# Kernel optimization log

Measured on AMD Instinct MI355X. Metric: run time of the kernel, lower is better.

The kernel has to match this reference:

```python
import jax, jax.numpy as jnp
import numpy as np

N_NODES = 50000


def gcn_conv(x, src, dst, W, b, n_nodes):
    """PyG-style GCNConv: x' = D^-1/2 (A + I) D^-1/2 (x W) + b.
    src/dst already include self-loops."""
    h = x @ W  # [N, C_out]
    # symmetric normalization from degree (with self-loops, unit edge weight)
    deg = jax.ops.segment_sum(jnp.ones_like(dst, dtype=h.dtype), dst,
                              num_segments=n_nodes)  # [N]
    dinv = jnp.where(deg > 0, jax.lax.rsqrt(deg), 0.0)
    norm = dinv[src] * dinv[dst]  # [E]
    msg = h[src] * norm[:, None]  # gather + scale, [E, C_out]
    out = jax.ops.segment_sum(msg, dst, num_segments=n_nodes)  # scatter-add
    return out + b


def setup_inputs() -> dict:
    key = jax.random.key(0)
    k1, k2, k3, k4, k5, k6 = jax.random.split(key, 6)
    in_c, hid_c, out_c = 128, 64, 64
    x = jax.random.normal(k1, (N_NODES, in_c), dtype=jnp.float32)
    edge_index = jax.random.randint(k2, (2, 800000), 0, N_NODES, dtype=jnp.int64)
    # Glorot-ish init for weights, zeros for bias (as PyG default)
    W1 = jax.random.normal(k3, (in_c, hid_c), dtype=jnp.float32) / np.sqrt(in_c)
    b1 = jnp.zeros((hid_c,), dtype=jnp.float32)
    W2 = jax.random.normal(k4, (hid_c, out_c), dtype=jnp.float32) / np.sqrt(hid_c)
    b2 = jnp.zeros((out_c,), dtype=jnp.float32)
    return {"x": x, "edge_index": edge_index, "W1": W1, "b1": b1,
            "W2": W2, "b2": b2}


def reference(x, edge_index, W1, b1, W2, b2):
    n = x.shape[0]
    loops = jnp.arange(n, dtype=edge_index.dtype)
    src = jnp.concatenate([edge_index[0], loops])  # add self-loops
    dst = jnp.concatenate([edge_index[1], loops])
    h = gcn_conv(x, src, dst, W1, b1, n)
    h = jax.nn.relu(h)
    return gcn_conv(h, src, dst, W2, b2, n)
```

## Files before the change

### kernel.cpp

```cpp
#include <hip/hip_runtime.h>
#include <hip/hip_fp16.h>


#define C_HID 64

static inline size_t alignup(size_t x) { return (x + 255) & ~(size_t)255; }

typedef __attribute__((address_space(3))) unsigned int lds_uint;
typedef __attribute__((address_space(1))) const unsigned int glob_uint;

__device__ __forceinline__ int blockScanIncl256(int v, int* wsum) {
    const int lane = threadIdx.x & 63, wav = threadIdx.x >> 6;
    int s = v;
#pragma unroll
    for (int off = 1; off < 64; off <<= 1) {
        int t = __shfl_up(s, off);
        if (lane >= off) s += t;
    }
    if (lane == 63) wsum[wav] = s;
    __syncthreads();
    if (wav == 0 && lane < 4) {
        int ws = wsum[lane];
#pragma unroll
        for (int off = 1; off < 4; off <<= 1) {
            int t = __shfl_up(ws, off);
            if (lane >= off) ws += t;
        }
        wsum[lane] = ws;
    }
    __syncthreads();
    return (wav ? wsum[wav - 1] : 0) + s;
}

template <int K>
__global__ __launch_bounds__(256) void gemm1_hist_kernel(
    const float* __restrict__ X, const float* __restrict__ W,
    const int* __restrict__ dst, __half* __restrict__ outh,
    int* __restrict__ S, int n, int E, int ePer, int nb) {
    constexpr int KP = K + 4;
    __shared__ float Xs[64 * KP];
    __shared__ float Ws[K * 64];
    __shared__ int h[256];
    const int t = threadIdx.x;
    const int lane = t & 63;
    const int wav = t >> 6;

    if ((int)blockIdx.x < nb) {
        h[t] = 0;
        __syncthreads();
        int beg = blockIdx.x * ePer, end = min(E, beg + ePer);
        for (int e = beg + t; e < end; e += 256)
            atomicAdd(&h[dst[e] >> 8], 1);
        __syncthreads();
        for (int b = t; b < nb; b += 256)
            S[(size_t)b * nb + blockIdx.x] = h[b];
        return;
    }

    const int row0 = ((int)blockIdx.x - nb) * 64;
    {
        const char* gb = (const char*)W;
        char* lb = (char*)Ws;
        for (int off = wav * 1024; off < K * 64 * 4; off += 4096)
            __builtin_amdgcn_global_load_lds((glob_uint*)(gb + off + lane * 16),
                                             (lds_uint*)(lb + off), 16, 0, 0);
    }
    if (row0 + 64 <= n) {
        const float4* g4 = (const float4*)(X + (size_t)row0 * K);
        for (int i = t; i < 64 * (K / 4); i += 256) {
            float4 v = g4[i];
            int r = i / (K / 4), k0 = (i % (K / 4)) * 4;
            *(float4*)&Xs[r * KP + k0] = v;
        }
    } else {
        for (int i = t; i < 64 * K; i += 256) {
            int r = i / K, k = i % K;
            Xs[r * KP + k] = (row0 + r < n) ? X[(size_t)(row0 + r) * K + k] : 0.0f;
        }
    }
    __syncthreads();

    const int tx = t & 15;
    const int ty = t >> 4;
    float acc[4][4] = {{0.f}};
#pragma unroll 2
    for (int k0 = 0; k0 < K; k0 += 4) {
        float4 a0 = *(const float4*)&Xs[(4 * ty + 0) * KP + k0];
        float4 a1 = *(const float4*)&Xs[(4 * ty + 1) * KP + k0];
        float4 a2 = *(const float4*)&Xs[(4 * ty + 2) * KP + k0];
        float4 a3 = *(const float4*)&Xs[(4 * ty + 3) * KP + k0];
        float4 b0 = *(const float4*)&Ws[(k0 + 0) * 64 + 4 * tx];
        float4 b1 = *(const float4*)&Ws[(k0 + 1) * 64 + 4 * tx];
        float4 b2 = *(const float4*)&Ws[(k0 + 2) * 64 + 4 * tx];
        float4 b3 = *(const float4*)&Ws[(k0 + 3) * 64 + 4 * tx];
        const float* ap[4] = {(const float*)&a0, (const float*)&a1,
                              (const float*)&a2, (const float*)&a3};
        const float* bp[4] = {(const float*)&b0, (const float*)&b1,
                              (const float*)&b2, (const float*)&b3};
#pragma unroll
        for (int r = 0; r < 4; ++r)
#pragma unroll
            for (int kk = 0; kk < 4; ++kk) {
                float av = ap[r][kk];
#pragma unroll
                for (int c = 0; c < 4; ++c)
                    acc[r][c] = fmaf(av, bp[kk][c], acc[r][c]);
            }
    }
#pragma unroll
    for (int r = 0; r < 4; ++r) {
        int row = row0 + 4 * ty + r;
        if (row < n) {
            __half2 p01 = __floats2half2_rn(acc[r][0], acc[r][1]);
            __half2 p23 = __floats2half2_rn(acc[r][2], acc[r][3]);
            float2 st;
            ((__half2*)&st)[0] = p01;
            ((__half2*)&st)[1] = p23;
            *(float2*)&outh[(size_t)row * 64 + 4 * tx] = st;
        }
    }
}

__global__ __launch_bounds__(256) void scan_rows_kernel(
    int* __restrict__ S, int* __restrict__ T, int nb) {
    __shared__ int wsum[4];
    const int b = blockIdx.x, t = threadIdx.x;
    int v = (t < nb) ? S[(size_t)b * nb + t] : 0;
    int incl = blockScanIncl256(v, wsum);
    if (t < nb) S[(size_t)b * nb + t] = incl - v;
    if (t == 0) T[b] = wsum[3];
}

__global__ __launch_bounds__(256) void scan_T_kernel(int* __restrict__ T, int nb) {
    __shared__ int wsum[4];
    const int t = threadIdx.x;
    int v = (t < nb) ? T[t] : 0;
    int incl = blockScanIncl256(v, wsum);
    if (t < nb) T[t] = incl - v;
    if (t == nb - 1) T[nb] = incl;
}

__global__ __launch_bounds__(256) void scatter_kernel(
    const int* __restrict__ src, const int* __restrict__ dst, int E, int ePer,
    const int* __restrict__ S, const int* __restrict__ T,
    unsigned* __restrict__ ebuf, int nb) {
    __shared__ int arr[256];
    const int b = blockIdx.x, t = threadIdx.x;
    if (t < nb) arr[t] = S[(size_t)t * nb + b] + T[t];
    __syncthreads();
    int beg = b * ePer, end = min(E, beg + ePer);
    for (int e = beg + t; e < end; e += 256) {
        int d = dst[e];
        int s = src[e];
        int pos = atomicAdd(&arr[d >> 8], 1);
        ebuf[pos] = ((unsigned)s << 8) | (unsigned)(d & 255);
    }
}

__global__ __launch_bounds__(256) void build_kernel(
    const unsigned* __restrict__ ebuf, const int* __restrict__ T,
    int* __restrict__ row_ptr, float* __restrict__ dinv,
    int* __restrict__ esrc, int n, int nb) {
    __shared__ int arr[256];
    __shared__ int wsum[4];
    const int b = blockIdx.x, t = threadIdx.x;
    const int node0 = b << 8;
    const int ebeg = T[b];
    const int eend = T[b + 1];

    arr[t] = 0;
    __syncthreads();
    for (int e = ebeg + t; e < eend; e += 256)
        atomicAdd(&arr[ebuf[e] & 255], 1);
    __syncthreads();
    int deg = arr[t];
    int incl = blockScanIncl256(deg, wsum);
    int excl = incl - deg;
    __syncthreads();
    arr[t] = ebeg + excl;
    int v = node0 + t;
    if (v < n) {
        row_ptr[v + 1] = ebeg + incl;
        dinv[v] = rsqrtf(1.0f + (float)deg);
        if (v == 0) row_ptr[0] = 0;
    }
    __syncthreads();
    for (int e = ebeg + t; e < eend; e += 256) {
        unsigned p = ebuf[e];
        int pos = atomicAdd(&arr[p & 255], 1);
        esrc[pos] = (int)(p >> 8);
    }
}

__global__ __launch_bounds__(256) void agg1_gemm2_kernel(
    const __half* __restrict__ g1, const int* __restrict__ row_ptr,
    const int* __restrict__ esrc, const float* __restrict__ dinv,
    const float* __restrict__ b1, const float* __restrict__ W2,
    __half* __restrict__ g2, int n) {
    __shared__ float Bt[64][68];
    __shared__ float Ws2[64 * 64];
    const int t = threadIdx.x, lane = t & 63, wav = t >> 6;

    {
        const char* gb = (const char*)W2;
        char* lb = (char*)Ws2;
        for (int off = wav * 1024; off < 64 * 64 * 4; off += 4096)
            __builtin_amdgcn_global_load_lds((glob_uint*)(gb + off + lane * 16),
                                             (lds_uint*)(lb + off), 16, 0, 0);
    }

    const int g = t >> 2;
    const int c = t & 3;
    const int row0 = blockIdx.x * 64;
    const int v = row0 + g;
    const float4* __restrict__ hs4 = (const float4*)g1;

    if (v < n) {
        float acc[16];
        float dv0 = dinv[v];
        {
            size_t rb = (size_t)v * 8 + 2 * c;
            float4 r0 = hs4[rb], r1 = hs4[rb + 1];
            const __half2* h0 = (const __half2*)&r0;
            const __half2* h1 = (const __half2*)&r1;
#pragma unroll
            for (int q = 0; q < 4; ++q) {
                float2 f0 = __half22float2(h0[q]);
                float2 f1 = __half22float2(h1[q]);
                acc[2 * q] = f0.x * dv0;     acc[2 * q + 1] = f0.y * dv0;
                acc[8 + 2 * q] = f1.x * dv0; acc[9 + 2 * q] = f1.y * dv0;
            }
        }
        const int beg = row_ptr[v], end = row_ptr[v + 1];
        int j = beg;
        for (; j + 2 <= end; j += 2) {
            int s0 = esrc[j], s1 = esrc[j + 1];
            float d0 = dinv[s0], d1 = dinv[s1];
            size_t rb0 = (size_t)s0 * 8 + 2 * c, rb1 = (size_t)s1 * 8 + 2 * c;
            float4 a0 = hs4[rb0], a1 = hs4[rb0 + 1];
            float4 e0 = hs4[rb1], e1 = hs4[rb1 + 1];
            const __half2* pa0 = (const __half2*)&a0;
            const __half2* pa1 = (const __half2*)&a1;
            const __half2* pe0 = (const __half2*)&e0;
            const __half2* pe1 = (const __half2*)&e1;
#pragma unroll
            for (int q = 0; q < 4; ++q) {
                float2 f;
                f = __half22float2(pa0[q]);
                acc[2 * q] = fmaf(f.x, d0, acc[2 * q]);
                acc[2 * q + 1] = fmaf(f.y, d0, acc[2 * q + 1]);
                f = __half22float2(pa1[q]);
                acc[8 + 2 * q] = fmaf(f.x, d0, acc[8 + 2 * q]);
                acc[9 + 2 * q] = fmaf(f.y, d0, acc[9 + 2 * q]);
                f = __half22float2(pe0[q]);
                acc[2 * q] = fmaf(f.x, d1, acc[2 * q]);
                acc[2 * q + 1] = fmaf(f.y, d1, acc[2 * q + 1]);
                f = __half22float2(pe1[q]);
                acc[8 + 2 * q] = fmaf(f.x, d1, acc[8 + 2 * q]);
                acc[9 + 2 * q] = fmaf(f.y, d1, acc[9 + 2 * q]);
            }
        }
        if (j < end) {
            int s0 = esrc[j];
            float d0 = dinv[s0];
            size_t rb0 = (size_t)s0 * 8 + 2 * c;
            float4 a0 = hs4[rb0], a1 = hs4[rb0 + 1];
            const __half2* pa0 = (const __half2*)&a0;
            const __half2* pa1 = (const __half2*)&a1;
#pragma unroll
            for (int q = 0; q < 4; ++q) {
                float2 f;
                f = __half22float2(pa0[q]);
                acc[2 * q] = fmaf(f.x, d0, acc[2 * q]);
                acc[2 * q + 1] = fmaf(f.y, d0, acc[2 * q + 1]);
                f = __half22float2(pa1[q]);
                acc[8 + 2 * q] = fmaf(f.x, d0, acc[8 + 2 * q]);
                acc[9 + 2 * q] = fmaf(f.y, d0, acc[9 + 2 * q]);
            }
        }
        const float* bb = b1 + c * 16;
#pragma unroll
        for (int u = 0; u < 4; ++u) {
            float4 w;
            w.x = fmaxf(fmaf(acc[4 * u + 0], dv0, bb[4 * u + 0]), 0.f);
            w.y = fmaxf(fmaf(acc[4 * u + 1], dv0, bb[4 * u + 1]), 0.f);
            w.z = fmaxf(fmaf(acc[4 * u + 2], dv0, bb[4 * u + 2]), 0.f);
            w.w = fmaxf(fmaf(acc[4 * u + 3], dv0, bb[4 * u + 3]), 0.f);
            *(float4*)&Bt[g][c * 16 + 4 * u] = w;
        }
    } else {
#pragma unroll
        for (int u = 0; u < 4; ++u)
            *(float4*)&Bt[g][c * 16 + 4 * u] = make_float4(0.f, 0.f, 0.f, 0.f);
    }
    __syncthreads();

    const int tx = t & 15;
    const int ty = t >> 4;
    float a2[4][4] = {{0.f}};
#pragma unroll 2
    for (int k0 = 0; k0 < 64; k0 += 4) {
        float4 x0 = *(const float4*)&Bt[4 * ty + 0][k0];
        float4 x1 = *(const float4*)&Bt[4 * ty + 1][k0];
        float4 x2 = *(const float4*)&Bt[4 * ty + 2][k0];
        float4 x3 = *(const float4*)&Bt[4 * ty + 3][k0];
        float4 w0 = *(const float4*)&Ws2[(k0 + 0) * 64 + 4 * tx];
        float4 w1 = *(const float4*)&Ws2[(k0 + 1) * 64 + 4 * tx];
        float4 w2 = *(const float4*)&Ws2[(k0 + 2) * 64 + 4 * tx];
        float4 w3 = *(const float4*)&Ws2[(k0 + 3) * 64 + 4 * tx];
        const float* xp[4] = {(const float*)&x0, (const float*)&x1,
                              (const float*)&x2, (const float*)&x3};
        const float* wp[4] = {(const float*)&w0, (const float*)&w1,
                              (const float*)&w2, (const float*)&w3};
#pragma unroll
        for (int r = 0; r < 4; ++r)
#pragma unroll
            for (int kk = 0; kk < 4; ++kk) {
                float av = xp[r][kk];
#pragma unroll
                for (int cc = 0; cc < 4; ++cc)
                    a2[r][cc] = fmaf(av, wp[kk][cc], a2[r][cc]);
            }
    }
#pragma unroll
    for (int r = 0; r < 4; ++r) {
        int row = row0 + 4 * ty + r;
        if (row < n) {
            float dv = dinv[row];
            __half2 p01 = __floats2half2_rn(a2[r][0] * dv, a2[r][1] * dv);
            __half2 p23 = __floats2half2_rn(a2[r][2] * dv, a2[r][3] * dv);
            float2 st;
            ((__half2*)&st)[0] = p01;
            ((__half2*)&st)[1] = p23;
            *(float2*)&g2[(size_t)row * 64 + 4 * tx] = st;
        }
    }
}

__global__ __launch_bounds__(256) void aggregate2_kernel(
    const __half* __restrict__ hs,
    const int* __restrict__ row_ptr,
    const int* __restrict__ esrc,
    const float* __restrict__ dinv,
    const float* __restrict__ bias,
    float* __restrict__ out, int n) {
    const int v = blockIdx.x * 32 + (threadIdx.x >> 3);
    if (v >= n) return;
    const int c8 = threadIdx.x & 7;
    const float4* __restrict__ hs4 = (const float4*)hs;

    const int beg = row_ptr[v];
    const int end = row_ptr[v + 1];

    float acc[8];
    {
        float4 raw = hs4[(size_t)v * 8 + c8];
        const __half2* hp = (const __half2*)&raw;
#pragma unroll
        for (int q = 0; q < 4; ++q) {
            float2 f = __half22float2(hp[q]);
            acc[2 * q] = f.x; acc[2 * q + 1] = f.y;
        }
    }

    int j = beg;
    for (; j + 4 <= end; j += 4) {
        int s0 = esrc[j], s1 = esrc[j + 1], s2 = esrc[j + 2], s3 = esrc[j + 3];
        float4 r0 = hs4[(size_t)s0 * 8 + c8];
        float4 r1 = hs4[(size_t)s1 * 8 + c8];
        float4 r2 = hs4[(size_t)s2 * 8 + c8];
        float4 r3 = hs4[(size_t)s3 * 8 + c8];
        const __half2* h0 = (const __half2*)&r0;
        const __half2* h1 = (const __half2*)&r1;
        const __half2* h2 = (const __half2*)&r2;
        const __half2* h3 = (const __half2*)&r3;
#pragma unroll
        for (int q = 0; q < 4; ++q) {
            float2 f0 = __half22float2(h0[q]);
            float2 f1 = __half22float2(h1[q]);
            float2 f2 = __half22float2(h2[q]);
            float2 f3 = __half22float2(h3[q]);
            acc[2 * q]     += (f0.x + f1.x) + (f2.x + f3.x);
            acc[2 * q + 1] += (f0.y + f1.y) + (f2.y + f3.y);
        }
    }
    for (; j < end; ++j) {
        int s0 = esrc[j];
        float4 r0 = hs4[(size_t)s0 * 8 + c8];
        const __half2* h0 = (const __half2*)&r0;
#pragma unroll
        for (int q = 0; q < 4; ++q) {
            float2 f0 = __half22float2(h0[q]);
            acc[2 * q] += f0.x;
            acc[2 * q + 1] += f0.y;
        }
    }

    float dv = dinv[v];
    float4 b0 = *(const float4*)(bias + c8 * 8);
    float4 b1v = *(const float4*)(bias + c8 * 8 + 4);
    float4 o0, o1;
    o0.x = fmaf(acc[0], dv, b0.x); o0.y = fmaf(acc[1], dv, b0.y);
    o0.z = fmaf(acc[2], dv, b0.z); o0.w = fmaf(acc[3], dv, b0.w);
    o1.x = fmaf(acc[4], dv, b1v.x); o1.y = fmaf(acc[5], dv, b1v.y);
    o1.z = fmaf(acc[6], dv, b1v.z); o1.w = fmaf(acc[7], dv, b1v.w);
    float4* op = (float4*)(out + (size_t)v * 64 + c8 * 8);
    op[0] = o0;
    op[1] = o1;
}

extern "C" void kernel_launch(void* const* d_in, const int* in_sizes, int n_in,
                              void* d_out, int out_size, void* d_ws, size_t ws_size,
                              hipStream_t stream) {
    const float* x  = (const float*)d_in[0];
    const int*   ei = (const int*)d_in[1];
    const float* W1 = (const float*)d_in[2];
    const float* b1 = (const float*)d_in[3];
    const float* W2 = (const float*)d_in[4];
    const float* b2 = (const float*)d_in[5];
    float* out = (float*)d_out;

    const int C_IN = 128;
    const int n = in_sizes[0] / C_IN;
    const int E = in_sizes[1] / 2;
    const int* src = ei;
    const int* dst = ei + E;

    const int nb = (n + 255) >> 8;
    const int ngb = (n + 63) / 64;
    const int ePer = (E + nb - 1) / nb;

    char* w = (char*)d_ws;
    float*    dinv    = (float*)w;    w += alignup((size_t)n * sizeof(float));
    __half*   g1      = (__half*)w;   w += alignup((size_t)n * C_HID * sizeof(__half));
    __half*   g2      = (__half*)w;   w += alignup((size_t)n * C_HID * sizeof(__half));
    int*      row_ptr = (int*)w;      w += alignup((size_t)(n + 1) * sizeof(int));
    int*      S       = (int*)w;      w += alignup((size_t)nb * nb * sizeof(int));
    int*      T       = (int*)w;      w += alignup((size_t)(nb + 1) * sizeof(int));
    unsigned* ebuf    = (unsigned*)w; w += alignup((size_t)E * sizeof(unsigned));
    int*      esrc    = (int*)w;

    gemm1_hist_kernel<128><<<nb + ngb, 256, 0, stream>>>(
        x, W1, dst, g1, S, n, E, ePer, nb);

    scan_rows_kernel<<<nb, 256, 0, stream>>>(S, T, nb);
    scan_T_kernel<<<1, 256, 0, stream>>>(T, nb);
    scatter_kernel<<<nb, 256, 0, stream>>>(src, dst, E, ePer, S, T, ebuf, nb);
    build_kernel<<<nb, 256, 0, stream>>>(ebuf, T, row_ptr, dinv, esrc, n, nb);

    agg1_gemm2_kernel<<<ngb, 256, 0, stream>>>(
        g1, row_ptr, esrc, dinv, b1, W2, g2, n);

    aggregate2_kernel<<<(n + 31) / 32, 256, 0, stream>>>(
        g2, row_ptr, esrc, dinv, b2, out, n);
}
```

Baseline: 162.4 us.

## Split aggregations into two column-half passes and unfuse layer-2 GEMM

Both neighbor aggregations now run in two passes over half of the feature columns, so each pass's gather set (64 B per node instead of 128 B) is more likely to stay in cache. The fused aggregate+GEMM2 kernel is split into a standalone aggregation writing relu output to an fp16 buffer and a separate GEMM kernel that reads it back. In exchange the change adds extra launches, re-reads edge lists and row pointers in each pass, and adds a round trip through global memory for the intermediate.

Measured after the change: 192.7 us. 18.6% more time.

```diff
diff --git a/kernel.cpp b/kernel.cpp
--- a/kernel.cpp
+++ b/kernel.cpp
@@ -192,134 +192,182 @@
     }
 }
 
-__global__ __launch_bounds__(256) void agg1_gemm2_kernel(
+__global__ __launch_bounds__(256) void agg1_half_kernel(
     const __half* __restrict__ g1, const int* __restrict__ row_ptr,
     const int* __restrict__ esrc, const float* __restrict__ dinv,
-    const float* __restrict__ b1, const float* __restrict__ W2,
-    __half* __restrict__ g2, int n) {
-    __shared__ float Bt[64][68];
-    __shared__ float Ws2[64 * 64];
-    const int t = threadIdx.x, lane = t & 63, wav = t >> 6;
-
+    const float* __restrict__ b1, __half* __restrict__ Bh, int n, int pass) {
+    const int v = blockIdx.x * 32 + (threadIdx.x >> 3);
+    if (v >= n) return;
+    const int c8 = threadIdx.x & 7;
+    const int cidx = pass * 8 + c8;
+    const float2* __restrict__ hs2 = (const float2*)g1;
+
+    float dv = dinv[v];
+    float a0, a1, a2, a3;
     {
-        const char* gb = (const char*)W2;
-        char* lb = (char*)Ws2;
-        for (int off = wav * 1024; off < 64 * 64 * 4; off += 4096)
+        float2 raw = hs2[(size_t)v * 16 + cidx];
+        const __half2* hp = (const __half2*)&raw;
+        float2 f0 = __half22float2(hp[0]), f1 = __half22float2(hp[1]);
+        a0 = f0.x * dv; a1 = f0.y * dv; a2 = f1.x * dv; a3 = f1.y * dv;
+    }
+    const int beg = row_ptr[v], end = row_ptr[v + 1];
+    int j = beg;
+    for (; j + 4 <= end; j += 4) {
+        int s0 = esrc[j], s1 = esrc[j + 1], s2 = esrc[j + 2], s3 = esrc[j + 3];
+        float d0 = dinv[s0], d1 = dinv[s1], d2 = dinv[s2], d3 = dinv[s3];
+        float2 r0 = hs2[(size_t)s0 * 16 + cidx];
+        float2 r1 = hs2[(size_t)s1 * 16 + cidx];
+        float2 r2 = hs2[(size_t)s2 * 16 + cidx];
+        float2 r3 = hs2[(size_t)s3 * 16 + cidx];
+        const __half2* h0 = (const __half2*)&r0;
+        const __half2* h1 = (const __half2*)&r1;
+        const __half2* h2 = (const __half2*)&r2;
+        const __half2* h3 = (const __half2*)&r3;
+        float2 f;
+        f = __half22float2(h0[0]); a0 = fmaf(f.x, d0, a0); a1 = fmaf(f.y, d0, a1);
+        f = __half22float2(h0[1]); a2 = fmaf(f.x, d0, a2); a3 = fmaf(f.y, d0, a3);
+        f = __half22float2(h1[0]); a0 = fmaf(f.x, d1, a0); a1 = fmaf(f.y, d1, a1);
+        f = __half22float2(h1[1]); a2 = fmaf(f.x, d1, a2); a3 = fmaf(f.y, d1, a3);
+        f = __half22float2(h2[0]); a0 = fmaf(f.x, d2, a0); a1 = fmaf(f.y, d2, a1);
+        f = __half22float2(h2[1]); a2 = fmaf(f.x, d2, a2); a3 = fmaf(f.y, d2, a3);
+        f = __half22float2(h3[0]); a0 = fmaf(f.x, d3, a0); a1 = fmaf(f.y, d3, a1);
+        f = __half22float2(h3[1]); a2 = fmaf(f.x, d3, a2); a3 = fmaf(f.y, d3, a3);
+    }
+    for (; j < end; ++j) {
+        int s0 = esrc[j];
+        float d0 = dinv[s0];
+        float2 r0 = hs2[(size_t)s0 * 16 + cidx];
+        const __half2* h0 = (const __half2*)&r0;
+        float2 f;
+        f = __half22float2(h0[0]); a0 = fmaf(f.x, d0, a0); a1 = fmaf(f.y, d0, a1);
+        f = __half22float2(h0[1]); a2 = fmaf(f.x, d0, a2); a3 = fmaf(f.y, d0, a3);
+    }
+    float4 b = *(const float4*)(b1 + cidx * 4);
+    float r0 = fmaxf(fmaf(a0, dv, b.x), 0.f);
+    float r1 = fmaxf(fmaf(a1, dv, b.y), 0.f);
+    float r2 = fmaxf(fmaf(a2, dv, b.z), 0.f);
+    float r3 = fmaxf(fmaf(a3, dv, b.w), 0.f);
+    float2 st;
+    ((__half2*)&st)[0] = __floats2half2_rn(r0, r1);
+    ((__half2*)&st)[1] = __floats2half2_rn(r2, r3);
+    ((float2*)Bh)[(size_t)v * 16 + cidx] = st;
+}
+
+__global__ __launch_bounds__(256) void agg2_half_kernel(
+    const __half* __restrict__ g2, const int* __restrict__ row_ptr,
+    const int* __restrict__ esrc, const float* __restrict__ dinv,
+    const float* __restrict__ b2, float* __restrict__ out, int n, int pass) {
+    const int v = blockIdx.x * 32 + (threadIdx.x >> 3);
+    if (v >= n) return;
+    const int c8 = threadIdx.x & 7;
+    const int cidx = pass * 8 + c8;
+    const float2* __restrict__ hs2 = (const float2*)g2;
+
+    float a0, a1, a2, a3;
+    {
+        float2 raw = hs2[(size_t)v * 16 + cidx];
+        const __half2* hp = (const __half2*)&raw;
+        float2 f0 = __half22float2(hp[0]), f1 = __half22float2(hp[1]);
+        a0 = f0.x; a1 = f0.y; a2 = f1.x; a3 = f1.y;
+    }
+    const int beg = row_ptr[v], end = row_ptr[v + 1];
+    int j = beg;
+    for (; j + 4 <= end; j += 4) {
+        int s0 = esrc[j], s1 = esrc[j + 1], s2 = esrc[j + 2], s3 = esrc[j + 3];
+        float2 r0 = hs2[(size_t)s0 * 16 + cidx];
+        float2 r1 = hs2[(size_t)s1 * 16 + cidx];
+        float2 r2 = hs2[(size_t)s2 * 16 + cidx];
+        float2 r3 = hs2[(size_t)s3 * 16 + cidx];
+        const __half2* h0 = (const __half2*)&r0;
+        const __half2* h1 = (const __half2*)&r1;
+        const __half2* h2 = (const __half2*)&r2;
+        const __half2* h3 = (const __half2*)&r3;
+        float2 f0 = __half22float2(h0[0]), g0 = __half22float2(h0[1]);
+        float2 f1 = __half22float2(h1[0]), g1v = __half22float2(h1[1]);
+        float2 f2 = __half22float2(h2[0]), g2v = __half22float2(h2[1]);
+        float2 f3 = __half22float2(h3[0]), g3 = __half22float2(h3[1]);
+        a0 += (f0.x + f1.x) + (f2.x + f3.x);
+        a1 += (f0.y + f1.y) + (f2.y + f3.y);
+        a2 += (g0.x + g1v.x) + (g2v.x + g3.x);
+        a3 += (g0.y + g1v.y) + (g2v.y + g3.y);
+    }
+    for (; j < end; ++j) {
+        int s0 = esrc[j];
+        float2 r0 = hs2[(size_t)s0 * 16 + cidx];
+        const __half2* h0 = (const __half2*)&r0;
+        float2 f = __half22float2(h0[0]), g = __half22float2(h0[1]);
+        a0 += f.x; a1 += f.y; a2 += g.x; a3 += g.y;
+    }
+    float dv = dinv[v];
+    float4 b = *(const float4*)(b2 + cidx * 4);
+    float4 o;
+    o.x = fmaf(a0, dv, b.x);
+    o.y = fmaf(a1, dv, b.y);
+    o.z = fmaf(a2, dv, b.z);
+    o.w = fmaf(a3, dv, b.w);
+    *(float4*)(out + (size_t)v * 64 + cidx * 4) = o;
+}
+
+__global__ __launch_bounds__(256) void gemm2_h_kernel(
+    const __half* __restrict__ Xh, const float* __restrict__ W,
+    const float* __restrict__ dinv, __half* __restrict__ outh, int n) {
+    constexpr int K = 64, KP = 68;
+    __shared__ float Xs[64 * KP];
+    __shared__ float Ws[K * 64];
+    const int t = threadIdx.x;
+    const int lane = t & 63;
+    const int wav = t >> 6;
+    const int row0 = blockIdx.x * 64;
+
+    {
+        const char* gb = (const char*)W;
+        char* lb = (char*)Ws;
+        for (int off = wav * 1024; off < K * 64 * 4; off += 4096)
             __builtin_amdgcn_global_load_lds((glob_uint*)(gb + off + lane * 16),
                                              (lds_uint*)(lb + off), 16, 0, 0);
     }
-
-    const int g = t >> 2;
-    const int c = t & 3;
-    const int row0 = blockIdx.x * 64;
-    const int v = row0 + g;
-    const float4* __restrict__ hs4 = (const float4*)g1;
-
-    if (v < n) {
-        float acc[16];
-        float dv0 = dinv[v];
-        {
-            size_t rb = (size_t)v * 8 + 2 * c;
-            float4 r0 = hs4[rb], r1 = hs4[rb + 1];
-            const __half2* h0 = (const __half2*)&r0;
-            const __half2* h1 = (const __half2*)&r1;
-#pragma unroll
-            for (int q = 0; q < 4; ++q) {
-                float2 f0 = __half22float2(h0[q]);
-                float2 f1 = __half22float2(h1[q]);
-                acc[2 * q] = f0.x * dv0;     acc[2 * q + 1] = f0.y * dv0;
-                acc[8 + 2 * q] = f1.x * dv0; acc[9 + 2 * q] = f1.y * dv0;
-            }
-        }
-        const int beg = row_ptr[v], end = row_ptr[v + 1];
-        int j = beg;
-        for (; j + 2 <= end; j += 2) {
-            int s0 = esrc[j], s1 = esrc[j + 1];
-            float d0 = dinv[s0], d1 = dinv[s1];
-            size_t rb0 = (size_t)s0 * 8 + 2 * c, rb1 = (size_t)s1 * 8 + 2 * c;
-            float4 a0 = hs4[rb0], a1 = hs4[rb0 + 1];
-            float4 e0 = hs4[rb1], e1 = hs4[rb1 + 1];
-            const __half2* pa0 = (const __half2*)&a0;
-            const __half2* pa1 = (const __half2*)&a1;
-            const __half2* pe0 = (const __half2*)&e0;
-            const __half2* pe1 = (const __half2*)&e1;
-#pragma unroll
-            for (int q = 0; q < 4; ++q) {
-                float2 f;
-                f = __half22float2(pa0[q]);
-                acc[2 * q] = fmaf(f.x, d0, acc[2 * q]);
-                acc[2 * q + 1] = fmaf(f.y, d0, acc[2 * q + 1]);
-                f = __half22float2(pa1[q]);
-                acc[8 + 2 * q] = fmaf(f.x, d0, acc[8 + 2 * q]);
-                acc[9 + 2 * q] = fmaf(f.y, d0, acc[9 + 2 * q]);
-                f = __half22float2(pe0[q]);
-                acc[2 * q] = fmaf(f.x, d1, acc[2 * q]);
-                acc[2 * q + 1] = fmaf(f.y, d1, acc[2 * q + 1]);
-                f = __half22float2(pe1[q]);
-                acc[8 + 2 * q] = fmaf(f.x, d1, acc[8 + 2 * q]);
-                acc[9 + 2 * q] = fmaf(f.y, d1, acc[9 + 2 * q]);
-            }
-        }
-        if (j < end) {
-            int s0 = esrc[j];
-            float d0 = dinv[s0];
-            size_t rb0 = (size_t)s0 * 8 + 2 * c;
-            float4 a0 = hs4[rb0], a1 = hs4[rb0 + 1];
-            const __half2* pa0 = (const __half2*)&a0;
-            const __half2* pa1 = (const __half2*)&a1;
-#pragma unroll
-            for (int q = 0; q < 4; ++q) {
-                float2 f;
-                f = __half22float2(pa0[q]);
-                acc[2 * q] = fmaf(f.x, d0, acc[2 * q]);
-                acc[2 * q + 1] = fmaf(f.y, d0, acc[2 * q + 1]);
-                f = __half22float2(pa1[q]);
-                acc[8 + 2 * q] = fmaf(f.x, d0, acc[8 + 2 * q]);
-                acc[9 + 2 * q] = fmaf(f.y, d0, acc[9 + 2 * q]);
-            }
-        }
-        const float* bb = b1 + c * 16;
-#pragma unroll
-        for (int u = 0; u < 4; ++u) {
-            float4 w;
-            w.x = fmaxf(fmaf(acc[4 * u + 0], dv0, bb[4 * u + 0]), 0.f);
-            w.y = fmaxf(fmaf(acc[4 * u + 1], dv0, bb[4 * u + 1]), 0.f);
-            w.z = fmaxf(fmaf(acc[4 * u + 2], dv0, bb[4 * u + 2]), 0.f);
-            w.w = fmaxf(fmaf(acc[4 * u + 3], dv0, bb[4 * u + 3]), 0.f);
-            *(float4*)&Bt[g][c * 16 + 4 * u] = w;
+    if (row0 + 64 <= n) {
+        const float2* g2p = (const float2*)(Xh + (size_t)row0 * 64);
+        for (int i = t; i < 64 * 16; i += 256) {
+            float2 raw = g2p[i];
+            const __half2* hp = (const __half2*)&raw;
+            float2 f0 = __half22float2(hp[0]), f1 = __half22float2(hp[1]);
+            int r = i >> 4, c4 = (i & 15) * 4;
+            *(float4*)&Xs[r * KP + c4] = make_float4(f0.x, f0.y, f1.x, f1.y);
         }
     } else {
-#pragma unroll
-        for (int u = 0; u < 4; ++u)
-            *(float4*)&Bt[g][c * 16 + 4 * u] = make_float4(0.f, 0.f, 0.f, 0.f);
+        for (int i = t; i < 64 * K; i += 256) {
+            int r = i / K, k = i % K;
+            Xs[r * KP + k] = (row0 + r < n) ? (float)Xh[(size_t)(row0 + r) * K + k] : 0.0f;
+        }
     }
     __syncthreads();
 
     const int tx = t & 15;
     const int ty = t >> 4;
-    float a2[4][4] = {{0.f}};
+    float acc[4][4] = {{0.f}};
 #pragma unroll 2
-    for (int k0 = 0; k0 < 64; k0 += 4) {
-        float4 x0 = *(const float4*)&Bt[4 * ty + 0][k0];
-        float4 x1 = *(const float4*)&Bt[4 * ty + 1][k0];
-        float4 x2 = *(const float4*)&Bt[4 * ty + 2][k0];
-        float4 x3 = *(const float4*)&Bt[4 * ty + 3][k0];
-        float4 w0 = *(const float4*)&Ws2[(k0 + 0) * 64 + 4 * tx];
-        float4 w1 = *(const float4*)&Ws2[(k0 + 1) * 64 + 4 * tx];
-        float4 w2 = *(const float4*)&Ws2[(k0 + 2) * 64 + 4 * tx];
-        float4 w3 = *(const float4*)&Ws2[(k0 + 3) * 64 + 4 * tx];
-        const float* xp[4] = {(const float*)&x0, (const float*)&x1,
-                              (const float*)&x2, (const float*)&x3};
-        const float* wp[4] = {(const float*)&w0, (const float*)&w1,
-                              (const float*)&w2, (const float*)&w3};
+    for (int k0 = 0; k0 < K; k0 += 4) {
+        float4 a0 = *(const float4*)&Xs[(4 * ty + 0) * KP + k0];
+        float4 a1 = *(const float4*)&Xs[(4 * ty + 1) * KP + k0];
+        float4 a2 = *(const float4*)&Xs[(4 * ty + 2) * KP + k0];
+        float4 a3 = *(const float4*)&Xs[(4 * ty + 3) * KP + k0];
+        float4 b0 = *(const float4*)&Ws[(k0 + 0) * 64 + 4 * tx];
+        float4 b1 = *(const float4*)&Ws[(k0 + 1) * 64 + 4 * tx];
+        float4 b2 = *(const float4*)&Ws[(k0 + 2) * 64 + 4 * tx];
+        float4 b3 = *(const float4*)&Ws[(k0 + 3) * 64 + 4 * tx];
+        const float* ap[4] = {(const float*)&a0, (const float*)&a1,
+                              (const float*)&a2, (const float*)&a3};
+        const float* bp[4] = {(const float*)&b0, (const float*)&b1,
+                              (const float*)&b2, (const float*)&b3};
 #pragma unroll
         for (int r = 0; r < 4; ++r)
 #pragma unroll
             for (int kk = 0; kk < 4; ++kk) {
-                float av = xp[r][kk];
-#pragma unroll
-                for (int cc = 0; cc < 4; ++cc)
-                    a2[r][cc] = fmaf(av, wp[kk][cc], a2[r][cc]);
+                float av = ap[r][kk];
+#pragma unroll
+                for (int c = 0; c < 4; ++c)
+                    acc[r][c] = fmaf(av, bp[kk][c], acc[r][c]);
             }
     }
 #pragma unroll
@@ -327,86 +375,14 @@
         int row = row0 + 4 * ty + r;
         if (row < n) {
             float dv = dinv[row];
-            __half2 p01 = __floats2half2_rn(a2[r][0] * dv, a2[r][1] * dv);
-            __half2 p23 = __floats2half2_rn(a2[r][2] * dv, a2[r][3] * dv);
+            __half2 p01 = __floats2half2_rn(acc[r][0] * dv, acc[r][1] * dv);
+            __half2 p23 = __floats2half2_rn(acc[r][2] * dv, acc[r][3] * dv);
             float2 st;
             ((__half2*)&st)[0] = p01;
             ((__half2*)&st)[1] = p23;
-            *(float2*)&g2[(size_t)row * 64 + 4 * tx] = st;
-        }
-    }
-}
-
-__global__ __launch_bounds__(256) void aggregate2_kernel(
-    const __half* __restrict__ hs,
-    const int* __restrict__ row_ptr,
-    const int* __restrict__ esrc,
-    const float* __restrict__ dinv,
-    const float* __restrict__ bias,
-    float* __restrict__ out, int n) {
-    const int v = blockIdx.x * 32 + (threadIdx.x >> 3);
-    if (v >= n) return;
-    const int c8 = threadIdx.x & 7;
-    const float4* __restrict__ hs4 = (const float4*)hs;
-
-    const int beg = row_ptr[v];
-    const int end = row_ptr[v + 1];
-
-    float acc[8];
-    {
-        float4 raw = hs4[(size_t)v * 8 + c8];
-        const __half2* hp = (const __half2*)&raw;
-#pragma unroll
-        for (int q = 0; q < 4; ++q) {
-            float2 f = __half22float2(hp[q]);
-            acc[2 * q] = f.x; acc[2 * q + 1] = f.y;
-        }
-    }
-
-    int j = beg;
-    for (; j + 4 <= end; j += 4) {
-        int s0 = esrc[j], s1 = esrc[j + 1], s2 = esrc[j + 2], s3 = esrc[j + 3];
-        float4 r0 = hs4[(size_t)s0 * 8 + c8];
-        float4 r1 = hs4[(size_t)s1 * 8 + c8];
-        float4 r2 = hs4[(size_t)s2 * 8 + c8];
-        float4 r3 = hs4[(size_t)s3 * 8 + c8];
-        const __half2* h0 = (const __half2*)&r0;
-        const __half2* h1 = (const __half2*)&r1;
-        const __half2* h2 = (const __half2*)&r2;
-        const __half2* h3 = (const __half2*)&r3;
-#pragma unroll
-        for (int q = 0; q < 4; ++q) {
-            float2 f0 = __half22float2(h0[q]);
-            float2 f1 = __half22float2(h1[q]);
-            float2 f2 = __half22float2(h2[q]);
-            float2 f3 = __half22float2(h3[q]);
-            acc[2 * q]     += (f0.x + f1.x) + (f2.x + f3.x);
-            acc[2 * q + 1] += (f0.y + f1.y) + (f2.y + f3.y);
-        }
-    }
-    for (; j < end; ++j) {
-        int s0 = esrc[j];
-        float4 r0 = hs4[(size_t)s0 * 8 + c8];
-        const __half2* h0 = (const __half2*)&r0;
-#pragma unroll
-        for (int q = 0; q < 4; ++q) {
-            float2 f0 = __half22float2(h0[q]);
-            acc[2 * q] += f0.x;
-            acc[2 * q + 1] += f0.y;
-        }
-    }
-
-    float dv = dinv[v];
-    float4 b0 = *(const float4*)(bias + c8 * 8);
-    float4 b1v = *(const float4*)(bias + c8 * 8 + 4);
-    float4 o0, o1;
-    o0.x = fmaf(acc[0], dv, b0.x); o0.y = fmaf(acc[1], dv, b0.y);
-    o0.z = fmaf(acc[2], dv, b0.z); o0.w = fmaf(acc[3], dv, b0.w);
-    o1.x = fmaf(acc[4], dv, b1v.x); o1.y = fmaf(acc[5], dv, b1v.y);
-    o1.z = fmaf(acc[6], dv, b1v.z); o1.w = fmaf(acc[7], dv, b1v.w);
-    float4* op = (float4*)(out + (size_t)v * 64 + c8 * 8);
-    op[0] = o0;
-    op[1] = o1;
+            *(float2*)&outh[(size_t)row * 64 + 4 * tx] = st;
+        }
+    }
 }
 
 extern "C" void kernel_launch(void* const* d_in, const int* in_sizes, int n_in,
@@ -428,11 +404,13 @@
 
     const int nb = (n + 255) >> 8;
     const int ngb = (n + 63) / 64;
+    const int nab = (n + 31) / 32;
     const int ePer = (E + nb - 1) / nb;
 
     char* w = (char*)d_ws;
     float*    dinv    = (float*)w;    w += alignup((size_t)n * sizeof(float));
     __half*   g1      = (__half*)w;   w += alignup((size_t)n * C_HID * sizeof(__half));
+    __half*   Bh      = (__half*)w;   w += alignup((size_t)n * C_HID * sizeof(__half));
     __half*   g2      = (__half*)w;   w += alignup((size_t)n * C_HID * sizeof(__half));
     int*      row_ptr = (int*)w;      w += alignup((size_t)(n + 1) * sizeof(int));
     int*      S       = (int*)w;      w += alignup((size_t)nb * nb * sizeof(int));
@@ -448,9 +426,11 @@
     scatter_kernel<<<nb, 256, 0, stream>>>(src, dst, E, ePer, S, T, ebuf, nb);
     build_kernel<<<nb, 256, 0, stream>>>(ebuf, T, row_ptr, dinv, esrc, n, nb);
 
-    agg1_gemm2_kernel<<<ngb, 256, 0, stream>>>(
-        g1, row_ptr, esrc, dinv, b1, W2, g2, n);
-
-    aggregate2_kernel<<<(n + 31) / 32, 256, 0, stream>>>(
-        g2, row_ptr, esrc, dinv, b2, out, n);
-}
+    agg1_half_kernel<<<nab, 256, 0, stream>>>(g1, row_ptr, esrc, dinv, b1, Bh, n, 0);
+    agg1_half_kernel<<<nab, 256, 0, stream>>>(g1, row_ptr, esrc, dinv, b1, Bh, n, 1);
+
+    gemm2_h_kernel<<<ngb, 256, 0, stream>>>(Bh, W2, dinv, g2, n);
+
+    agg2_half_kernel<<<nab, 256, 0, stream>>>(g2, row_ptr, esrc, dinv, b2, out, n, 0);
+    agg2_half_kernel<<<nab, 256, 0, stream>>>(g2, row_ptr, esrc, dinv, b2, out, n, 1);
+}
```
